# Performance work log

Measured on AMD Instinct MI355X. Metric: run time of the kernel, lower is better.

## Reference

```python
import jax, jax.numpy as jnp
import numpy as np
from jax import lax

N_SAMPLES = 64
POS_PER_BATCH = 16  # round(64 * 0.25)
POS_IOU = 0.5
EXCL_IOU = 0.1
IMG_H = 1024.0
IMG_W = 1024.0
BBOX_STD = jnp.array([0.1, 0.1, 0.2, 0.2], dtype=jnp.float32)
EPS = 1e-7


def _iou_matrix(rois, gts):
    # rois (R,4), gts (G,4) in (y1,x1,y2,x2) -> (R,G)
    y1 = jnp.maximum(rois[:, None, 0], gts[None, :, 0])
    x1 = jnp.maximum(rois[:, None, 1], gts[None, :, 1])
    y2 = jnp.minimum(rois[:, None, 2], gts[None, :, 2])
    x2 = jnp.minimum(rois[:, None, 3], gts[None, :, 3])
    inter = jnp.clip(y2 - y1, 0.0) * jnp.clip(x2 - x1, 0.0)
    area_r = jnp.clip(rois[:, 2] - rois[:, 0], 0.0) * jnp.clip(rois[:, 3] - rois[:, 1], 0.0)
    area_g = jnp.clip(gts[:, 2] - gts[:, 0], 0.0) * jnp.clip(gts[:, 3] - gts[:, 1], 0.0)
    union = area_r[:, None] + area_g[None, :] - inter
    return inter / jnp.maximum(union, EPS)


def _get_offsets(rois, gts):
    rh = jnp.maximum(rois[:, 2] - rois[:, 0], EPS)
    rw = jnp.maximum(rois[:, 3] - rois[:, 1], EPS)
    rcy = rois[:, 0] + 0.5 * rh
    rcx = rois[:, 1] + 0.5 * rw
    gh = jnp.maximum(gts[:, 2] - gts[:, 0], EPS)
    gw = jnp.maximum(gts[:, 3] - gts[:, 1], EPS)
    gcy = gts[:, 0] + 0.5 * gh
    gcx = gts[:, 1] + 0.5 * gw
    return jnp.stack([(gcy - rcy) / rh, (gcx - rcx) / rw,
                      jnp.log(gh / rh), jnp.log(gw / rw)], axis=-1)


def _per_image(roi, gt_bbox_n, gt_label):
    # roi (R,4) normalized; gt_bbox_n (G,4) normalized; gt_label (G,)
    roi_valid = jnp.any(roi != 0, axis=1)
    gt_valid = jnp.any(gt_bbox_n != 0, axis=1)
    ious = _iou_matrix(roi, gt_bbox_n)           # (R,G)
    ious = jnp.where(gt_valid[None, :], ious, -1.0)
    max_iou = ious.max(axis=1)
    idx_max_gt = ious.argmax(axis=1)

    pos = roi_valid & (max_iou >= POS_IOU)
    neg = roi_valid & (max_iou < POS_IOU) & (max_iou >= EXCL_IOU)
    R = roi.shape[0]
    ar = jnp.arange(R)
    # deterministic subsample (lowest index first) in place of tf.random_shuffle
    _, pos_idx = lax.top_k(jnp.where(pos, R - ar, 0), POS_PER_BATCH)
    _, neg_idx = lax.top_k(jnp.where(neg, R - ar, 0), N_SAMPLES)
    n_pos = jnp.minimum(pos.sum(), POS_PER_BATCH)
    n_neg = jnp.minimum(neg.sum(), N_SAMPLES - n_pos)

    slots = jnp.arange(N_SAMPLES)
    is_pos = slots < n_pos
    is_neg = (slots >= n_pos) & (slots < n_pos + n_neg)
    valid = is_pos | is_neg
    pidx = pos_idx[jnp.clip(slots, 0, POS_PER_BATCH - 1)]
    nidx = neg_idx[jnp.clip(slots - n_pos, 0, N_SAMPLES - 1)]
    ridx = jnp.where(is_pos, pidx, jnp.where(is_neg, nidx, 0))

    s_roi_raw = roi[ridx]                        # (64,4)
    gidx = idx_max_gt[ridx]
    s_gt = gt_bbox_n[gidx]
    vf = valid.astype(roi.dtype)[:, None]
    s_roi = s_roi_raw * vf
    s_off = (_get_offsets(s_roi_raw, s_gt) * vf) / BBOX_STD
    s_lab = jnp.where(is_pos, gt_label[gidx], 0).astype(jnp.int32)
    return s_roi, s_off, s_lab


def _forward(normalized_rois, gt_bboxes, gt_labels):
    gt_norm = gt_bboxes / jnp.array([IMG_H, IMG_W, IMG_H, IMG_W], dtype=gt_bboxes.dtype)
    return jax.vmap(_per_image)(normalized_rois, gt_norm, gt_labels)


def setup_inputs() -> dict:
    key = jax.random.key(0)
    k1, k2, k3, k4, k5, k6 = jax.random.split(key, 6)
    B, R, G = 8, 20000, 256
    cy = jax.random.uniform(k1, (B, G)) * IMG_H
    cx = jax.random.uniform(k2, (B, G)) * IMG_W
    sz = jax.random.uniform(k3, (B, G, 2)) * 180.0 + 20.0
    y1 = jnp.clip(cy - 0.5 * sz[..., 0], 0, IMG_H)
    y2 = jnp.clip(cy + 0.5 * sz[..., 0], 0, IMG_H)
    x1 = jnp.clip(cx - 0.5 * sz[..., 1], 0, IMG_W)
    x2 = jnp.clip(cx + 0.5 * sz[..., 1], 0, IMG_W)
    gt_bboxes = jnp.stack([y1, x1, y2, x2], axis=-1).astype(jnp.float32)
    gt_labels = jax.random.randint(k4, (B, G), 1, 81, dtype=jnp.int32)
    gt_norm = gt_bboxes / jnp.array([IMG_H, IMG_W, IMG_H, IMG_W], dtype=jnp.float32)
    # jittered copies of gt boxes guarantee positive RoIs
    jit = jnp.clip(jnp.tile(gt_norm, (1, 4, 1)) + 0.02 * jax.random.normal(k5, (B, 4 * G, 4)), 0.0, 1.0)
    rc = jax.random.uniform(k6, (B, R - 4 * G, 4))
    ry1 = jnp.minimum(rc[..., 0], rc[..., 2]); ry2 = jnp.maximum(rc[..., 0], rc[..., 2])
    rx1 = jnp.minimum(rc[..., 1], rc[..., 3]); rx2 = jnp.maximum(rc[..., 1], rc[..., 3])
    rand_rois = jnp.stack([ry1, rx1, ry2, rx2], axis=-1)
    normalized_rois = jnp.concatenate([jit, rand_rois], axis=1).astype(jnp.float32)
    return {"normalized_rois": normalized_rois, "gt_bboxes": gt_bboxes, "gt_labels": gt_labels}


def reference(normalized_rois, gt_bboxes, gt_labels):
    return _forward(normalized_rois, gt_bboxes, gt_labels)
```

## Files before the change

kernel.cpp:

```cpp
#include <hip/hip_runtime.h>

#pragma clang fp contract(off)

#define GMAX 256
#define K1B 128

__device__ __forceinline__ unsigned int ordf(float f) {
    unsigned int u = __float_as_uint(f);
    return (u & 0x80000000u) ? ~u : (u | 0x80000000u);
}

__global__ __launch_bounds__(K1B) void iou_cls_kernel(
    const float* __restrict__ rois, const float* __restrict__ gts,
    unsigned long long* __restrict__ pmask, unsigned long long* __restrict__ nmask,
    int R, int G, int NW)
{
    const int bi = blockIdx.y;
    const int r  = blockIdx.x * K1B + threadIdx.x;

    __shared__ float4 gbox[GMAX];
    __shared__ float  garea[GMAX];

    for (int t = threadIdx.x; t < G; t += K1B) {
        const float4 g4 = *reinterpret_cast<const float4*>(gts + ((size_t)bi * G + t) * 4);
        const float s = 1.0f / 1024.0f;
        float a = g4.x * s, b = g4.y * s, c = g4.z * s, d = g4.w * s;
        const bool valid = (a != 0.f) || (b != 0.f) || (c != 0.f) || (d != 0.f);
        if (!valid) { a = 4.f; b = 4.f; c = 4.f; d = 4.f; }
        gbox[t]  = make_float4(a, b, c, d);
        garea[t] = valid ? fmaxf(c - a, 0.f) * fmaxf(d - b, 0.f) : 0.0f;
    }
    __syncthreads();
    if (r >= R) return;

    const float4 rr = *reinterpret_cast<const float4*>(rois + ((size_t)bi * R + r) * 4);
    const bool rv = (rr.x != 0.f) || (rr.y != 0.f) || (rr.z != 0.f) || (rr.w != 0.f);
    const float ar = fmaxf(rr.z - rr.x, 0.f) * fmaxf(rr.w - rr.y, 0.f);

    float best = 0.0f;
    #pragma unroll 4
    for (int g = 0; g < G; ++g) {
        const float4 gb = gbox[g];
        const float y1 = fmaxf(rr.x, gb.x);
        const float x1 = fmaxf(rr.y, gb.y);
        const float y2 = fminf(rr.z, gb.z);
        const float x2 = fminf(rr.w, gb.w);
        const float inter = fmaxf(y2 - y1, 0.f) * fmaxf(x2 - x1, 0.f);
        const float uni   = (ar + garea[g]) - inter;
        const float iou   = inter / fmaxf(uni, 1e-7f);
        best = fmaxf(best, iou);
    }

    const bool pos = rv && (best >= 0.5f);
    const bool neg = rv && !(best >= 0.5f) && (best >= 0.1f);

    const unsigned long long bp = __ballot(pos);
    const unsigned long long bn = __ballot(neg);
    const int w = r >> 6;
    if ((threadIdx.x & 63) == 0 && w < NW) {
        pmask[(size_t)bi * NW + w] = bp;
        nmask[(size_t)bi * NW + w] = bn;
    }
}

__global__ __launch_bounds__(512) void select_kernel(
    const float* __restrict__ rois, const float* __restrict__ gts,
    const int* __restrict__ labels,
    const unsigned long long* __restrict__ pmask, const unsigned long long* __restrict__ nmask,
    float* __restrict__ out, int R, int G, int B, int NW)
{
    const int bi  = blockIdx.x;
    const int tid = threadIdx.x;

    __shared__ int sp[512], sn[512];
    __shared__ float4 sgt[GMAX];
    __shared__ float  sgv[GMAX];
    __shared__ int plist[16], nlist[64];
    __shared__ int sridx[64];
    __shared__ unsigned long long skey[64];

    for (int t = tid; t < G; t += 512) {
        const float4 g4 = *reinterpret_cast<const float4*>(gts + ((size_t)bi * G + t) * 4);
        const float s = 1.0f / 1024.0f;
        const float a = g4.x * s, b = g4.y * s, c = g4.z * s, d = g4.w * s;
        sgt[t] = make_float4(a, b, c, d);
        sgv[t] = ((a != 0.f) || (b != 0.f) || (c != 0.f) || (d != 0.f)) ? 1.0f : 0.0f;
    }

    unsigned long long mp = 0ull, mn = 0ull;
    if (tid < NW) {
        mp = pmask[(size_t)bi * NW + tid];
        mn = nmask[(size_t)bi * NW + tid];
    }
    const int cp = __popcll(mp);
    const int cn = __popcll(mn);
    sp[tid] = cp; sn[tid] = cn;
    if (tid < 16) plist[tid] = 0;
    if (tid < 64) nlist[tid] = 0;
    __syncthreads();
    for (int off = 1; off < 512; off <<= 1) {
        const int vp = (tid >= off) ? sp[tid - off] : 0;
        const int vn = (tid >= off) ? sn[tid - off] : 0;
        __syncthreads();
        sp[tid] += vp; sn[tid] += vn;
        __syncthreads();
    }
    const int basep = sp[tid] - cp;
    const int basen = sn[tid] - cn;

    if (mp && basep < 16) {
        int rank = basep; unsigned long long m = mp;
        while (m && rank < 16) { const int b = __ffsll(m) - 1; plist[rank++] = tid * 64 + b; m &= m - 1; }
    }
    if (mn && basen < 64) {
        int rank = basen; unsigned long long m = mn;
        while (m && rank < 64) { const int b = __ffsll(m) - 1; nlist[rank++] = tid * 64 + b; m &= m - 1; }
    }
    __syncthreads();

    const int tot_p = sp[511];
    const int tot_n = sn[511];
    const int n_pos = min(tot_p, 16);
    const int n_neg = min(tot_n, 64 - n_pos);

    if (tid < 64) {
        const int slot = tid;
        const bool isp = slot < n_pos;
        const bool isn = (!isp) && (slot < n_pos + n_neg);
        sridx[slot] = isp ? plist[slot] : (isn ? nlist[slot - n_pos] : 0);
        skey[slot]  = 0ull;
    }
    __syncthreads();

    {
        const int slot = tid >> 3;
        const int sub  = tid & 7;
        const int ridx = sridx[slot];
        const float4 rr = *reinterpret_cast<const float4*>(rois + ((size_t)bi * R + ridx) * 4);
        const float ar = fmaxf(rr.z - rr.x, 0.f) * fmaxf(rr.w - rr.y, 0.f);
        float best = -1.0f;
        int bidx = sub * 32;
        for (int j = 0; j < 32; ++j) {
            const int g = sub * 32 + j;
            if (g >= G) break;
            const float4 gb = sgt[g];
            const float y1 = fmaxf(rr.x, gb.x);
            const float x1 = fmaxf(rr.y, gb.y);
            const float y2 = fminf(rr.z, gb.z);
            const float x2 = fminf(rr.w, gb.w);
            const float inter = fmaxf(y2 - y1, 0.f) * fmaxf(x2 - x1, 0.f);
            const float ga = fmaxf(gb.z - gb.x, 0.f) * fmaxf(gb.w - gb.y, 0.f);
            const float uni = (ar + ga) - inter;
            float v = inter / fmaxf(uni, 1e-7f);
            if (sgv[g] == 0.0f) v = -1.0f;
            if (v > best) { best = v; bidx = g; }
        }
        const unsigned long long key =
            ((unsigned long long)ordf(best) << 32) | (unsigned int)(~(unsigned int)bidx);
        atomicMax(&skey[slot], key);
    }
    __syncthreads();

    if (tid < 64) {
        const int slot = tid;
        const bool isp = slot < n_pos;
        const bool isn = (!isp) && (slot < n_pos + n_neg);
        const int ridx = sridx[slot];
        const int gidx = (int)(~(unsigned int)(skey[slot] & 0xFFFFFFFFull));

        const float4 rr = *reinterpret_cast<const float4*>(rois + ((size_t)bi * R + ridx) * 4);
        const float4 gb = sgt[gidx];
        const float vf = (isp || isn) ? 1.0f : 0.0f;
        const float eps = 1e-7f;

        const float rh  = fmaxf(rr.z - rr.x, eps);
        const float rw  = fmaxf(rr.w - rr.y, eps);
        const float rcy = rr.x + 0.5f * rh;
        const float rcx = rr.y + 0.5f * rw;
        const float gh  = fmaxf(gb.z - gb.x, eps);
        const float gw  = fmaxf(gb.w - gb.y, eps);
        const float gcy = gb.x + 0.5f * gh;
        const float gcx = gb.y + 0.5f * gw;

        float o0 = (gcy - rcy) / rh;
        float o1 = (gcx - rcx) / rw;
        float o2 = logf(gh / rh);
        float o3 = logf(gw / rw);
        o0 = (o0 * vf) / 0.1f;
        o1 = (o1 * vf) / 0.1f;
        o2 = (o2 * vf) / 0.2f;
        o3 = (o3 * vf) / 0.2f;

        const int base = bi * 64 + slot;
        reinterpret_cast<float4*>(out)[base] = make_float4(rr.x * vf, rr.y * vf, rr.z * vf, rr.w * vf);
        reinterpret_cast<float4*>(out + (size_t)B * 256)[base] = make_float4(o0, o1, o2, o3);
        out[(size_t)B * 512 + base] = isp ? (float)labels[(size_t)bi * G + gidx] : 0.0f;
    }
}

extern "C" void kernel_launch(void* const* d_in, const int* in_sizes, int n_in,
                              void* d_out, int out_size, void* d_ws, size_t ws_size,
                              hipStream_t stream)
{
    const float* rois   = (const float*)d_in[0];
    const float* gts    = (const float*)d_in[1];
    const int*   labels = (const int*)d_in[2];
    float* out = (float*)d_out;

    const int B = out_size / 576;
    const int G = in_sizes[2] / B;
    const int R = in_sizes[0] / (4 * B);
    const int NW = (R + 63) / 64;

    unsigned long long* pmask = (unsigned long long*)d_ws;
    unsigned long long* nmask = pmask + (size_t)B * NW;

    dim3 gridA((R + K1B - 1) / K1B, B);
    iou_cls_kernel<<<gridA, K1B, 0, stream>>>(rois, gts, pmask, nmask, R, G, NW);
    select_kernel<<<B, 512, 0, stream>>>(rois, gts, labels, pmask, nmask, out, R, G, B, NW);
}
```

Measured before the change: 121.9 us.

## Split GT loop across four waves and replace IoU division with threshold compares

The IoU classification kernel now uses 256-thread blocks, with each of the four waves scanning a quarter of the (padded to 256) GT boxes for the same 64 RoIs. Per-wave ballots are OR-combined through shared memory. The per-pair float division and max are replaced by double-precision comparisons of inter against union scaled by constants chosen to reproduce the float thresholds 0.5 and 0.1. This removes the serial divide chain and increases parallelism per RoI. In exchange it adds double-precision multiplies, always loops over the full GMAX boxes even when G is smaller, and depends on the constants matching float rounding exactly.

```diff
diff --git a/kernel.cpp b/kernel.cpp
--- a/kernel.cpp
+++ b/kernel.cpp
@@ -3,43 +3,55 @@
 #pragma clang fp contract(off)
 
 #define GMAX 256
-#define K1B 128
 
 __device__ __forceinline__ unsigned int ordf(float f) {
     unsigned int u = __float_as_uint(f);
     return (u & 0x80000000u) ? ~u : (u | 0x80000000u);
 }
 
-__global__ __launch_bounds__(K1B) void iou_cls_kernel(
+__global__ __launch_bounds__(256) void iou_cls_kernel(
     const float* __restrict__ rois, const float* __restrict__ gts,
     unsigned long long* __restrict__ pmask, unsigned long long* __restrict__ nmask,
     int R, int G, int NW)
 {
-    const int bi = blockIdx.y;
-    const int r  = blockIdx.x * K1B + threadIdx.x;
+    const int bi    = blockIdx.y;
+    const int lane  = threadIdx.x & 63;
+    const int gbase = threadIdx.x & 192;
+    const int r     = blockIdx.x * 64 + lane;
 
     __shared__ float4 gbox[GMAX];
     __shared__ float  garea[GMAX];
-
-    for (int t = threadIdx.x; t < G; t += K1B) {
-        const float4 g4 = *reinterpret_cast<const float4*>(gts + ((size_t)bi * G + t) * 4);
-        const float s = 1.0f / 1024.0f;
-        float a = g4.x * s, b = g4.y * s, c = g4.z * s, d = g4.w * s;
-        const bool valid = (a != 0.f) || (b != 0.f) || (c != 0.f) || (d != 0.f);
-        if (!valid) { a = 4.f; b = 4.f; c = 4.f; d = 4.f; }
+    __shared__ unsigned long long bp[4], ba[4];
+
+    for (int t = threadIdx.x; t < GMAX; t += 256) {
+        float a = 4.f, b = 4.f, c = 4.f, d = 4.f, area = 0.f;
+        if (t < G) {
+            const float4 g4 = *reinterpret_cast<const float4*>(gts + ((size_t)bi * G + t) * 4);
+            const float s = 1.0f / 1024.0f;
+            const float na = g4.x * s, nb = g4.y * s, nc = g4.z * s, nd = g4.w * s;
+            if ((na != 0.f) || (nb != 0.f) || (nc != 0.f) || (nd != 0.f)) {
+                a = na; b = nb; c = nc; d = nd;
+                area = fmaxf(nc - na, 0.f) * fmaxf(nd - nb, 0.f);
+            }
+        }
         gbox[t]  = make_float4(a, b, c, d);
-        garea[t] = valid ? fmaxf(c - a, 0.f) * fmaxf(d - b, 0.f) : 0.0f;
-    }
-    __syncthreads();
-    if (r >= R) return;
-
-    const float4 rr = *reinterpret_cast<const float4*>(rois + ((size_t)bi * R + r) * 4);
-    const bool rv = (rr.x != 0.f) || (rr.y != 0.f) || (rr.z != 0.f) || (rr.w != 0.f);
+        garea[t] = area;
+    }
+    __syncthreads();
+
+    float4 rr = make_float4(0.f, 0.f, 0.f, 0.f);
+    if (r < R) rr = *reinterpret_cast<const float4*>(rois + ((size_t)bi * R + r) * 4);
+    const bool rv = (r < R) &&
+        ((rr.x != 0.f) || (rr.y != 0.f) || (rr.z != 0.f) || (rr.w != 0.f));
     const float ar = fmaxf(rr.z - rr.x, 0.f) * fmaxf(rr.w - rr.y, 0.f);
 
-    float best = 0.0f;
+    const double C1 = 33554431.0 / 67108864.0;
+    const double C2 = 26843545.0 / 268435456.0;
+    bool anyp = false, any1 = false;
+
     #pragma unroll 4
-    for (int g = 0; g < G; ++g) {
+    for (int j = 0; j < 64; ++j) {
+        const int g = gbase + j;
         const float4 gb = gbox[g];
         const float y1 = fmaxf(rr.x, gb.x);
         const float x1 = fmaxf(rr.y, gb.y);
@@ -47,19 +59,24 @@
         const float x2 = fminf(rr.w, gb.w);
         const float inter = fmaxf(y2 - y1, 0.f) * fmaxf(x2 - x1, 0.f);
         const float uni   = (ar + garea[g]) - inter;
-        const float iou   = inter / fmaxf(uni, 1e-7f);
-        best = fmaxf(best, iou);
-    }
-
-    const bool pos = rv && (best >= 0.5f);
-    const bool neg = rv && !(best >= 0.5f) && (best >= 0.1f);
-
-    const unsigned long long bp = __ballot(pos);
-    const unsigned long long bn = __ballot(neg);
-    const int w = r >> 6;
-    if ((threadIdx.x & 63) == 0 && w < NW) {
-        pmask[(size_t)bi * NW + w] = bp;
-        nmask[(size_t)bi * NW + w] = bn;
+        const float uni2  = fmaxf(uni, 1e-7f);
+        const double A = (double)inter;
+        const double B = (double)uni2;
+        anyp = anyp | (A >= C1 * B);
+        any1 = any1 | (A >  C2 * B);
+    }
+
+    const int wave = threadIdx.x >> 6;
+    const unsigned long long brv = __ballot(rv);
+    bp[wave] = __ballot(anyp);
+    ba[wave] = __ballot(any1);
+    __syncthreads();
+
+    if (threadIdx.x == 0) {
+        const unsigned long long por = bp[0] | bp[1] | bp[2] | bp[3];
+        const unsigned long long aor = ba[0] | ba[1] | ba[2] | ba[3];
+        pmask[(size_t)bi * NW + blockIdx.x] = brv & por;
+        nmask[(size_t)bi * NW + blockIdx.x] = brv & aor & ~por;
     }
 }
 
@@ -215,7 +232,7 @@
     unsigned long long* pmask = (unsigned long long*)d_ws;
     unsigned long long* nmask = pmask + (size_t)B * NW;
 
-    dim3 gridA((R + K1B - 1) / K1B, B);
-    iou_cls_kernel<<<gridA, K1B, 0, stream>>>(rois, gts, pmask, nmask, R, G, NW);
+    dim3 gridA(NW, B);
+    iou_cls_kernel<<<gridA, 256, 0, stream>>>(rois, gts, pmask, nmask, R, G, NW);
     select_kernel<<<B, 512, 0, stream>>>(rois, gts, labels, pmask, nmask, out, R, G, B, NW);
 }
```

Result: faster. 97.85 us (-19.7%).
